# Kernel tuning notes

Measured on AMD Instinct MI355X. Metric: run time of the kernel, lower is better.

Reference implementation:

```python
import jax, jax.numpy as jnp
import numpy as np
from jax import lax

# dims
B_SZ, H_SZ, W_SZ = 2, 48, 48
D_MODEL = 192
SSM_RATIO = 2.0
D_PROJ = int(SSM_RATIO * D_MODEL)        # 384
C_INNER = 2 * D_PROJ                     # 768 = K * D_IN
K_GRP = 4
D_IN = C_INNER // K_GRP                  # 192 (= d_inner, channel_divide=2)
N_STATE = 16
R_RANK = 12                              # ceil(192/16)


def setup_inputs() -> dict:
    key = jax.random.key(0)
    ks = jax.random.split(key, 12)
    x = jax.random.normal(ks[0], (B_SZ, H_SZ, W_SZ, 2 * D_MODEL), jnp.float32)
    in_proj_w = jax.random.normal(ks[1], (C_INNER, 2 * D_MODEL), jnp.float32) * 0.02
    conv_w = jax.random.normal(ks[2], (C_INNER, 1, 3, 3), jnp.float32) * 0.1
    conv_b = jnp.zeros((C_INNER,), jnp.float32)
    x_proj_weight = jax.random.normal(ks[3], (K_GRP, R_RANK + 2 * N_STATE, D_IN), jnp.float32) * 0.05
    dt_projs_weight = jax.random.normal(ks[4], (K_GRP, D_IN, R_RANK), jnp.float32) * (R_RANK ** -0.5)
    # faithful dt bias init: softplus^{-1}(dt) with dt ~ logU[1e-3, 1e-1]
    dt = jnp.exp(jax.random.uniform(ks[5], (K_GRP, D_IN)) * (np.log(0.1) - np.log(0.001)) + np.log(0.001))
    dt = jnp.clip(dt, 1e-4, None)
    dt_projs_bias = dt + jnp.log(-jnp.expm1(-dt))
    # A_log init: log(arange(1..N)) per channel, K copies merged
    A_logs = jnp.log(jnp.tile(jnp.arange(1, N_STATE + 1, dtype=jnp.float32)[None, :], (K_GRP * D_IN, 1)))
    Ds = jnp.ones((K_GRP * D_IN,), jnp.float32)
    out_norm_w = jnp.ones((C_INNER,), jnp.float32)
    out_norm_b = jnp.zeros((C_INNER,), jnp.float32)
    out_proj_w = jax.random.normal(ks[6], (2 * D_MODEL, C_INNER), jnp.float32) * 0.02
    return dict(x=x, in_proj_w=in_proj_w, conv_w=conv_w, conv_b=conv_b,
                x_proj_weight=x_proj_weight, dt_projs_weight=dt_projs_weight,
                dt_projs_bias=dt_projs_bias, A_logs=A_logs, Ds=Ds,
                out_norm_w=out_norm_w, out_norm_b=out_norm_b, out_proj_w=out_proj_w)


def _ss2d(x, in_proj_w, conv_w, conv_b, x_proj_weight, dt_projs_weight,
          dt_projs_bias, A_logs, Ds, out_norm_w, out_norm_b, out_proj_w):
    B, H, W, _ = x.shape
    C = in_proj_w.shape[0]
    K = x_proj_weight.shape[0]
    d = C // K
    N = A_logs.shape[1]
    R = dt_projs_weight.shape[2]
    L = H * W

    # in_proj (disable_z: no gating split)
    xz = jnp.einsum('bhwc,oc->bhwo', x, in_proj_w)
    xc = xz.transpose(0, 3, 1, 2)  # [B,C,H,W]
    # depthwise 3x3 conv + SiLU
    xc = lax.conv_general_dilated(xc, conv_w, (1, 1), 'SAME', feature_group_count=C)
    xc = xc + conv_b[None, :, None, None]
    xc = xc * jax.nn.sigmoid(xc)

    # CrossScanS: split channels into K groups, each scanned in its own direction
    ch = xc.reshape(B, K, d, H, W)
    f0 = ch[:, 0].reshape(B, d, L)                                        # row-major fwd
    f1 = ch[:, 1].transpose(0, 1, 3, 2).reshape(B, d, L)                  # col-major fwd
    f2 = jnp.flip(ch[:, 2].reshape(B, d, L), -1)                          # row-major rev
    f3 = jnp.flip(ch[:, 3].transpose(0, 1, 3, 2).reshape(B, d, L), -1)    # col-major rev
    xs = jnp.stack([f0, f1, f2, f3], axis=1)  # [B,K,d,L]

    # input-dependent dt/B/C projections
    x_dbl = jnp.einsum('bkdl,kcd->bkcl', xs, x_proj_weight)
    dts, Bs, Cs = jnp.split(x_dbl, [R, R + N], axis=2)  # [B,K,R,L],[B,K,N,L],[B,K,N,L]
    dts = jnp.einsum('bkrl,kdr->bkdl', dts, dt_projs_weight) + dt_projs_bias[None, :, :, None]

    # force_fp32 selective scan with delta_softplus
    u = xs.astype(jnp.float32)
    dts = jax.nn.softplus(dts.astype(jnp.float32))
    Bs = Bs.astype(jnp.float32)
    Cs = Cs.astype(jnp.float32)
    A = -jnp.exp(A_logs.astype(jnp.float32)).reshape(K, d, N)  # [K,d,N]

    def step(h, inp):
        u_t, dt_t, B_t, C_t = inp  # [B,K,d],[B,K,d],[B,K,N],[B,K,N]
        h = h * jnp.exp(dt_t[..., None] * A) + (dt_t * u_t)[..., None] * B_t[:, :, None, :]
        y_t = jnp.einsum('bkdn,bkn->bkd', h, C_t)
        return h, y_t

    inps = (u.transpose(3, 0, 1, 2), dts.transpose(3, 0, 1, 2),
            Bs.transpose(3, 0, 1, 2), Cs.transpose(3, 0, 1, 2))
    h0 = jnp.zeros((B, K, d, N), jnp.float32)
    _, ys = lax.scan(step, h0, inps)          # ys: [L,B,K,d]
    ys = ys.transpose(1, 2, 3, 0)             # [B,K,d,L]
    ys = ys + Ds.astype(jnp.float32).reshape(K, d)[None, :, :, None] * u

    # CrossMergeS: undo each direction, concat channels back
    y0 = ys[:, 0]
    y1 = ys[:, 1].reshape(B, d, W, H).transpose(0, 1, 3, 2).reshape(B, d, L)
    y2 = jnp.flip(ys[:, 2], -1)
    y3 = jnp.flip(ys[:, 3], -1).reshape(B, d, W, H).transpose(0, 1, 3, 2).reshape(B, d, L)
    y = jnp.concatenate([y0, y1, y2, y3], axis=1).reshape(B, C, H, W).transpose(0, 2, 3, 1)

    # out_norm: LayerNorm over channels
    mu = jnp.mean(y, -1, keepdims=True)
    var = jnp.mean(jnp.square(y - mu), -1, keepdims=True)
    y = (y - mu) * lax.rsqrt(var + 1e-5) * out_norm_w + out_norm_b

    out = jnp.einsum('bhwc,oc->bhwo', y.astype(x.dtype), out_proj_w)
    return out


def reference(x, in_proj_w, conv_w, conv_b, x_proj_weight, dt_projs_weight,
              dt_projs_bias, A_logs, Ds, out_norm_w, out_norm_b, out_proj_w):
    return _ss2d(x, in_proj_w, conv_w, conv_b, x_proj_weight, dt_projs_weight,
                 dt_projs_bias, A_logs, Ds, out_norm_w, out_norm_b, out_proj_w)
```

## Files before the change

kernel.cpp:

```cpp
#include <hip/hip_runtime.h>
#include <hip/hip_bf16.h>

#define B_SZ   2
#define H_SZ   48
#define W_SZ   48
#define L_SZ   2304
#define CIN    768
#define KG     4
#define DI     192
#define NS     16
#define RR     12
#define XD     44
#define MTOK   4608
#define CL     16
#define NC     144

typedef __attribute__((ext_vector_type(8))) short short8;
typedef __attribute__((ext_vector_type(4))) float f32x4;

__device__ inline ushort f2b(float f) {
    uint u = __builtin_bit_cast(uint, f);
    u = (u + 0x7FFF + ((u >> 16) & 1)) >> 16;
    return (ushort)u;
}
__device__ inline float b2f(ushort b) {
    uint u = ((uint)b) << 16;
    return __builtin_bit_cast(float, u);
}
__device__ inline short8 f2b8(float4 a, float4 b) {
    short8 r;
    r[0] = (short)f2b(a.x); r[1] = (short)f2b(a.y);
    r[2] = (short)f2b(a.z); r[3] = (short)f2b(a.w);
    r[4] = (short)f2b(b.x); r[5] = (short)f2b(b.y);
    r[6] = (short)f2b(b.z); r[7] = (short)f2b(b.w);
    return r;
}

template<int TM, bool ABF, bool CBF>
__global__ __launch_bounds__(256) void gemm_tn64(
        const void* __restrict__ Av, const float* __restrict__ Bw,
        void* __restrict__ Cv, int M, int N, int K) {
    __shared__ ushort As[TM][40];
    __shared__ ushort Bs[64][40];
    const int tid  = threadIdx.x;
    const int lane = tid & 63;
    const int wave = tid >> 6;
    constexpr int MF = TM / 64;
    const int wrow = wave * (MF * 16);
    const int bm = blockIdx.y * TM, bn = blockIdx.x * 64;
    const int frow = lane & 15;
    const int fk   = (lane >> 4) * 8;
    const int orow = (lane >> 4) * 4;

    f32x4 acc[MF][4] = {};

    for (int k0 = 0; k0 < K; k0 += 32) {
        short8 aval[MF];
#pragma unroll
        for (int i = 0; i < MF; ++i) {
            int idx = tid + i * 256;
            int row = idx >> 2, q = idx & 3;
            if (ABF) {
                aval[i] = *(const short8*)&((const ushort*)Av)[(size_t)(bm + row) * K + k0 + q * 8];
            } else {
                const float* ap = &((const float*)Av)[(size_t)(bm + row) * K + k0 + q * 8];
                aval[i] = f2b8(*(const float4*)ap, *(const float4*)(ap + 4));
            }
        }
        const float* bp = &Bw[(size_t)(bn + (tid >> 2)) * K + k0 + (tid & 3) * 8];
        short8 bval = f2b8(*(const float4*)bp, *(const float4*)(bp + 4));

        __syncthreads();
#pragma unroll
        for (int i = 0; i < MF; ++i) {
            int idx = tid + i * 256;
            *(short8*)&As[idx >> 2][(idx & 3) * 8] = aval[i];
        }
        *(short8*)&Bs[tid >> 2][(tid & 3) * 8] = bval;
        __syncthreads();

        short8 af[MF], bf[4];
#pragma unroll
        for (int mi = 0; mi < MF; ++mi)
            af[mi] = *(const short8*)&As[wrow + mi * 16 + frow][fk];
#pragma unroll
        for (int ni = 0; ni < 4; ++ni)
            bf[ni] = *(const short8*)&Bs[ni * 16 + frow][fk];
#pragma unroll
        for (int mi = 0; mi < MF; ++mi)
#pragma unroll
            for (int ni = 0; ni < 4; ++ni)
                acc[mi][ni] = __builtin_amdgcn_mfma_f32_16x16x32_bf16(
                                  af[mi], bf[ni], acc[mi][ni], 0, 0, 0);
    }

#pragma unroll
    for (int mi = 0; mi < MF; ++mi) {
        int rbase = bm + wrow + mi * 16 + orow;
#pragma unroll
        for (int ni = 0; ni < 4; ++ni) {
            int col = bn + ni * 16 + frow;
#pragma unroll
            for (int r = 0; r < 4; ++r) {
                if (CBF)
                    ((ushort*)Cv)[(size_t)(rbase + r) * N + col] = f2b(acc[mi][ni][r]);
                else
                    ((float*)Cv)[(size_t)(rbase + r) * N + col] = acc[mi][ni][r];
            }
        }
    }
}

__global__ __launch_bounds__(256) void conv_silu_scatter(
        const ushort* __restrict__ xzb, const float* __restrict__ cw,
        const float* __restrict__ cb, ushort* __restrict__ xsb) {
    int idx = blockIdx.x * 256 + threadIdx.x;
    int c = idx % CIN;
    int rest = idx / CIN;
    int w = rest % W_SZ; rest /= W_SZ;
    int h = rest % H_SZ;
    int b = rest / H_SZ;

    float acc = cb[c];
#pragma unroll
    for (int dh = -1; dh <= 1; ++dh) {
        int hh = h + dh;
        if (hh < 0 || hh >= H_SZ) continue;
#pragma unroll
        for (int dw = -1; dw <= 1; ++dw) {
            int ww = w + dw;
            if (ww < 0 || ww >= W_SZ) continue;
            acc += b2f(xzb[(size_t)((b * H_SZ + hh) * W_SZ + ww) * CIN + c])
                 * cw[c * 9 + (dh + 1) * 3 + (dw + 1)];
        }
    }
    float s = acc * __builtin_amdgcn_rcpf(1.f + __expf(-acc));

    int k = c / DI, d = c % DI;
    int lrow = h * W_SZ + w;
    int lcol = w * H_SZ + h;
    int l;
    if      (k == 0) l = lrow;
    else if (k == 1) l = lcol;
    else if (k == 2) l = L_SZ - 1 - lrow;
    else             l = L_SZ - 1 - lcol;
    xsb[(size_t)((b * KG + k) * L_SZ + l) * DI + d] = f2b(s);
}

__global__ __launch_bounds__(384) void xproj_dt_mfma(
        const ushort* __restrict__ xsb, const float* __restrict__ xpw,
        const float* __restrict__ dtw, const float* __restrict__ dtb,
        float* __restrict__ xdbl, ushort* __restrict__ dts_b) {
    __shared__ ushort Ws[48][200];
    __shared__ ushort Wd[192][40];
    __shared__ ushort dsh[32][40];

    const int tid  = threadIdx.x;
    const int lane = tid & 63;
    const int wave = tid >> 6;
    const int bm = blockIdx.x * 32;
    const int bk = blockIdx.y;
    const int k  = bk & 3;
    const int frow = lane & 15;
    const int fk   = (lane >> 4) * 8;
    const int orow = (lane >> 4) * 4;
    const int rg = wave & 1;
    const int cg = wave >> 1;

#pragma unroll
    for (int i = 0; i < 6; ++i) {
        int idx = tid + i * 384;
        int row = idx / 48, g = idx % 48;
        ushort4 u = {0, 0, 0, 0};
        if (row < XD) {
            float4 v = *(const float4*)&xpw[((size_t)(k * XD) + row) * 192 + g * 4];
            u.x = f2b(v.x); u.y = f2b(v.y); u.z = f2b(v.z); u.w = f2b(v.w);
        }
        *(ushort4*)&Ws[row][g * 4] = u;
    }
#pragma unroll
    for (int i = 0; i < 3; ++i) {
        int idx = tid + i * 384;
        if (idx < 960) {
            float4 z = {0.f, 0.f, 0.f, 0.f};
            *(float4*)&Wd[idx / 5][(idx % 5) * 8] = z;
        } else if (idx < 1120) {
            int j = idx - 960;
            float4 z = {0.f, 0.f, 0.f, 0.f};
            *(float4*)&dsh[j / 5][(j % 5) * 8] = z;
        }
    }
    __syncthreads();

#pragma unroll
    for (int i = 0; i < 6; ++i) {
        int idx = tid + i * 384;
        int row = idx / RR, c = idx % RR;
        Wd[row][c] = f2b(dtw[((size_t)(k * DI) + row) * RR + c]);
    }

    f32x4 acc1 = {};
    const ushort* arow = &xsb[(size_t)(bk * L_SZ + bm + rg * 16 + frow) * DI];
#pragma unroll
    for (int k0 = 0; k0 < 192; k0 += 32) {
        short8 af = *(const short8*)&arow[k0 + fk];
        short8 bv = *(const short8*)&Ws[cg * 16 + frow][k0 + fk];
        acc1 = __builtin_amdgcn_mfma_f32_16x16x32_bf16(af, bv, acc1, 0, 0, 0);
    }

    {
        int col = cg * 16 + frow;
#pragma unroll
        for (int r = 0; r < 4; ++r) {
            float v = acc1[r];
            int row = rg * 16 + orow + r;
            if (col >= RR && col < XD)
                xdbl[(size_t)(bk * L_SZ + bm + row) * XD + col] = v;
            if (cg == 0 && col < RR)
                dsh[row][col] = f2b(v);
        }
    }
    __syncthreads();

#pragma unroll
    for (int t = 0; t < 2; ++t) {
        int d = (wave * 2 + t) * 16 + frow;
        short8 bv = *(const short8*)&Wd[d][fk];
        float bias = dtb[k * DI + d];
#pragma unroll
        for (int rg2 = 0; rg2 < 2; ++rg2) {
            short8 af2 = *(const short8*)&dsh[rg2 * 16 + frow][fk];
            f32x4 a2 = {};
            a2 = __builtin_amdgcn_mfma_f32_16x16x32_bf16(af2, bv, a2, 0, 0, 0);
#pragma unroll
            for (int r = 0; r < 4; ++r) {
                float a = a2[r] + bias;
                float sp = fmaxf(a, 0.f) + __logf(1.f + __expf(-fabsf(a)));
                dts_b[(size_t)(bk * L_SZ + bm + rg2 * 16 + orow + r) * DI + d] = f2b(sp);
            }
        }
    }
}

__global__ __launch_bounds__(192) void scan_passA(
        const ushort* __restrict__ dts_b, const ushort* __restrict__ xsb,
        const float* __restrict__ xdbl, const float* __restrict__ A_logs,
        float* __restrict__ Ebuf, float* __restrict__ Sbuf) {
    int blk = blockIdx.x;
    int bk = blk / NC, ch = blk % NC;
    int d = threadIdx.x, k = bk % KG;
    int l0 = ch * CL;

    __shared__ float bsh[CL][NS];
    for (int t = threadIdx.x; t < CL * NS; t += 192) {
        int l = t / NS, n = t % NS;
        bsh[l][n] = xdbl[(size_t)(bk * L_SZ + l0 + l) * XD + RR + n];
    }
    __syncthreads();

    float Aa[NS], E[NS], S[NS];
    const float* ar = &A_logs[(size_t)(k * DI + d) * NS];
    bool fast = true;
#pragma unroll
    for (int n = 0; n < NS; ++n) {
        Aa[n] = -__expf(ar[n]);
        E[n] = 1.f; S[n] = 0.f;
        fast = fast && (fabsf(Aa[n] + (float)(n + 1)) < 1e-4f * (n + 1));
    }

    if (fast) {
        float P = 1.f;
#pragma unroll 4
        for (int l = 0; l < CL; ++l) {
            float dt = b2f(dts_b[(size_t)(bk * L_SZ + l0 + l) * DI + d]);
            float u  = b2f(xsb [(size_t)(bk * L_SZ + l0 + l) * DI + d]);
            float du = dt * u;
            float4 b0 = *(const float4*)&bsh[l][0];
            float4 b1 = *(const float4*)&bsh[l][4];
            float4 b2 = *(const float4*)&bsh[l][8];
            float4 b3 = *(const float4*)&bsh[l][12];
            float Bv[NS] = {b0.x,b0.y,b0.z,b0.w, b1.x,b1.y,b1.z,b1.w,
                            b2.x,b2.y,b2.z,b2.w, b3.x,b3.y,b3.z,b3.w};
            float e1 = __expf(-dt);
            P *= e1;
            float e = e1;
            S[0] = fmaf(S[0], e, du * Bv[0]);
#pragma unroll
            for (int n = 1; n < NS; ++n) {
                e *= e1;
                S[n] = fmaf(S[n], e, du * Bv[n]);
            }
        }
        E[0] = P;
#pragma unroll
        for (int n = 1; n < NS; ++n) E[n] = E[n - 1] * P;
    } else {
#pragma unroll 4
        for (int l = 0; l < CL; ++l) {
            float dt = b2f(dts_b[(size_t)(bk * L_SZ + l0 + l) * DI + d]);
            float u  = b2f(xsb [(size_t)(bk * L_SZ + l0 + l) * DI + d]);
            float du = dt * u;
            float4 b0 = *(const float4*)&bsh[l][0];
            float4 b1 = *(const float4*)&bsh[l][4];
            float4 b2 = *(const float4*)&bsh[l][8];
            float4 b3 = *(const float4*)&bsh[l][12];
            float Bv[NS] = {b0.x,b0.y,b0.z,b0.w, b1.x,b1.y,b1.z,b1.w,
                            b2.x,b2.y,b2.z,b2.w, b3.x,b3.y,b3.z,b3.w};
#pragma unroll
            for (int n = 0; n < NS; ++n) {
                float e = __expf(dt * Aa[n]);
                E[n] *= e;
                S[n] = fmaf(S[n], e, du * Bv[n]);
            }
        }
    }
    float* ep = &Ebuf[(size_t)((bk * NC + ch) * DI + d) * NS];
    float* sp = &Sbuf[(size_t)((bk * NC + ch) * DI + d) * NS];
#pragma unroll
    for (int n = 0; n < NS; ++n) { ep[n] = E[n]; sp[n] = S[n]; }
}

__global__ __launch_bounds__(64) void scan_passB(
        const float* __restrict__ Ebuf, const float* __restrict__ Sbuf,
        float* __restrict__ Hstart) {
    constexpr int P = 8;
    int t = blockIdx.x * 64 + threadIdx.x;
    int bk = t / (DI * 4);
    int dn = (t % (DI * 4)) * 4;
    const size_t stride = (size_t)DI * NS;
    size_t off  = (size_t)(bk * NC) * stride + dn;
    size_t offL = off;

    float4 eA[P], sA[P], eB[P], sB[P];
    float4 h = {0.f, 0.f, 0.f, 0.f};

#pragma unroll
    for (int j = 0; j < P; ++j) {
        eA[j] = *(const float4*)&Ebuf[offL + (size_t)j * stride];
        sA[j] = *(const float4*)&Sbuf[offL + (size_t)j * stride];
    }
    offL += (size_t)P * stride;

    for (int c = 0; c < NC; c += 2 * P) {
#pragma unroll
        for (int j = 0; j < P; ++j) {
            eB[j] = *(const float4*)&Ebuf[offL + (size_t)j * stride];
            sB[j] = *(const float4*)&Sbuf[offL + (size_t)j * stride];
        }
        offL += (size_t)P * stride;

#pragma unroll
        for (int j = 0; j < P; ++j) {
            *(float4*)&Hstart[off + (size_t)j * stride] = h;
            h.x = fmaf(eA[j].x, h.x, sA[j].x);
            h.y = fmaf(eA[j].y, h.y, sA[j].y);
            h.z = fmaf(eA[j].z, h.z, sA[j].z);
            h.w = fmaf(eA[j].w, h.w, sA[j].w);
        }
        off += (size_t)P * stride;

        if (c + 2 * P < NC) {
#pragma unroll
            for (int j = 0; j < P; ++j) {
                eA[j] = *(const float4*)&Ebuf[offL + (size_t)j * stride];
                sA[j] = *(const float4*)&Sbuf[offL + (size_t)j * stride];
            }
        }
        offL += (size_t)P * stride;

#pragma unroll
        for (int j = 0; j < P; ++j) {
            *(float4*)&Hstart[off + (size_t)j * stride] = h;
            h.x = fmaf(eB[j].x, h.x, sB[j].x);
            h.y = fmaf(eB[j].y, h.y, sB[j].y);
            h.z = fmaf(eB[j].z, h.z, sB[j].z);
            h.w = fmaf(eB[j].w, h.w, sB[j].w);
        }
        off += (size_t)P * stride;
    }
}

__global__ __launch_bounds__(192) void scan_passC(
        const ushort* __restrict__ dts_b, const ushort* __restrict__ xsb,
        const float* __restrict__ xdbl, const float* __restrict__ A_logs,
        const float* __restrict__ Hstart, const float* __restrict__ Ds,
        ushort* __restrict__ ypre_b) {
    int blk = blockIdx.x;
    int bk = blk / NC, ch = blk % NC;
    int d = threadIdx.x, k = bk % KG, b = bk / KG;
    int l0 = ch * CL;

    __shared__ float bsh[CL][NS];
    __shared__ float csh[CL][NS];
    for (int t = threadIdx.x; t < CL * NS; t += 192) {
        int l = t / NS, n = t % NS;
        const float* row = &xdbl[(size_t)(bk * L_SZ + l0 + l) * XD];
        bsh[l][n] = row[RR + n];
        csh[l][n] = row[RR + NS + n];
    }
    __syncthreads();

    float Aa[NS], h[NS];
    const float* ar = &A_logs[(size_t)(k * DI + d) * NS];
    const float* hp = &Hstart[(size_t)((bk * NC + ch) * DI + d) * NS];
    bool fast = true;
#pragma unroll
    for (int n = 0; n < NS; ++n) {
        Aa[n] = -__expf(ar[n]);
        h[n] = hp[n];
        fast = fast && (fabsf(Aa[n] + (float)(n + 1)) < 1e-4f * (n + 1));
    }
    float Dd = Ds[k * DI + d];

#pragma unroll 4
    for (int l = 0; l < CL; ++l) {
        float dt = b2f(dts_b[(size_t)(bk * L_SZ + l0 + l) * DI + d]);
        float u  = b2f(xsb [(size_t)(bk * L_SZ + l0 + l) * DI + d]);
        float du = dt * u;
        float4 b0 = *(const float4*)&bsh[l][0];
        float4 b1 = *(const float4*)&bsh[l][4];
        float4 b2 = *(const float4*)&bsh[l][8];
        float4 b3 = *(const float4*)&bsh[l][12];
        float Bv[NS] = {b0.x,b0.y,b0.z,b0.w, b1.x,b1.y,b1.z,b1.w,
                        b2.x,b2.y,b2.z,b2.w, b3.x,b3.y,b3.z,b3.w};
        float4 c0 = *(const float4*)&csh[l][0];
        float4 c1 = *(const float4*)&csh[l][4];
        float4 c2 = *(const float4*)&csh[l][8];
        float4 c3 = *(const float4*)&csh[l][12];
        float Cv[NS] = {c0.x,c0.y,c0.z,c0.w, c1.x,c1.y,c1.z,c1.w,
                        c2.x,c2.y,c2.z,c2.w, c3.x,c3.y,c3.z,c3.w};
        float p[NS];
        if (fast) {
            float e1 = __expf(-dt);
            float e = e1;
            h[0] = fmaf(h[0], e, du * Bv[0]);
            p[0] = h[0] * Cv[0];
#pragma unroll
            for (int n = 1; n < NS; ++n) {
                e *= e1;
                h[n] = fmaf(h[n], e, du * Bv[n]);
                p[n] = h[n] * Cv[n];
            }
        } else {
#pragma unroll
            for (int n = 0; n < NS; ++n) {
                float e = __expf(dt * Aa[n]);
                h[n] = fmaf(h[n], e, du * Bv[n]);
                p[n] = h[n] * Cv[n];
            }
        }
#pragma unroll
        for (int s = 8; s >= 1; s >>= 1)
#pragma unroll
            for (int n = 0; n < 8; ++n)
                if (n < s) p[n] = p[n] + p[n + s];
        float y = fmaf(Dd, u, p[0]);

        int lg = l0 + l;
        int pos;
        if      (k == 0) pos = lg;
        else if (k == 1) pos = (lg % H_SZ) * W_SZ + (lg / H_SZ);
        else if (k == 2) pos = L_SZ - 1 - lg;
        else { int j = L_SZ - 1 - lg; pos = (j % H_SZ) * W_SZ + (j / H_SZ); }
        ypre_b[(size_t)(b * L_SZ + pos) * CIN + k * DI + d] = f2b(y);
    }
}

__global__ __launch_bounds__(256) void layernorm_bf16(
        const ushort* __restrict__ y, ushort* __restrict__ yb,
        const float* __restrict__ w, const float* __restrict__ bg) {
    int wave = threadIdx.x >> 6, lane = threadIdx.x & 63;
    int tok = blockIdx.x * 4 + wave;
    const ushort* row = &y[(size_t)tok * CIN];
    ushort* rowo = &yb[(size_t)tok * CIN];
    float v[12];
    float s = 0.f;
#pragma unroll
    for (int i = 0; i < 12; ++i) { v[i] = b2f(row[lane + i * 64]); s += v[i]; }
#pragma unroll
    for (int off = 32; off >= 1; off >>= 1) s += __shfl_xor(s, off, 64);
    float mu = s * (1.f / CIN);
    float s2 = 0.f;
#pragma unroll
    for (int i = 0; i < 12; ++i) { float t = v[i] - mu; s2 += t * t; }
#pragma unroll
    for (int off = 32; off >= 1; off >>= 1) s2 += __shfl_xor(s2, off, 64);
    float rstd = rsqrtf(s2 * (1.f / CIN) + 1e-5f);
#pragma unroll
    for (int i = 0; i < 12; ++i)
        rowo[lane + i * 64] =
            f2b((v[i] - mu) * rstd * w[lane + i * 64] + bg[lane + i * 64]);
}

extern "C" void kernel_launch(void* const* d_in, const int* in_sizes, int n_in,
                              void* d_out, int out_size, void* d_ws, size_t ws_size,
                              hipStream_t stream) {
    const float* x    = (const float*)d_in[0];
    const float* inw  = (const float*)d_in[1];
    const float* cw   = (const float*)d_in[2];
    const float* cb   = (const float*)d_in[3];
    const float* xpw  = (const float*)d_in[4];
    const float* dtw  = (const float*)d_in[5];
    const float* dtb  = (const float*)d_in[6];
    const float* alog = (const float*)d_in[7];
    const float* Dsp  = (const float*)d_in[8];
    const float* lnw  = (const float*)d_in[9];
    const float* lnb  = (const float*)d_in[10];
    const float* outw = (const float*)d_in[11];
    float* out = (float*)d_out;

    float* ws = (float*)d_ws;
    const size_t SZ_BIG = (size_t)MTOK * CIN;
    const size_t SCAN_SL = (size_t)8 * NC * DI * NS;
    float* xz    = ws;
    float* xsbf  = xz  + SZ_BIG;
    float* dts   = xsbf + SZ_BIG / 2;
    float* xdbl  = dts + SZ_BIG;
    float* Ebuf  = xdbl + (size_t)8 * L_SZ * XD;
    float* Sbuf  = Ebuf + SCAN_SL;
    float* Hst   = Sbuf + SCAN_SL;
    ushort* xzb    = (ushort*)xz;
    ushort* xsb    = (ushort*)xsbf;
    ushort* dtsb   = (ushort*)dts;
    ushort* ypre_b = (ushort*)xz;
    ushort* ynrm_b = (ushort*)dts;

    gemm_tn64<128, false, true><<<dim3(CIN / 64, MTOK / 128), 256, 0, stream>>>(
        x, inw, xzb, MTOK, CIN, 384);
    conv_silu_scatter<<<(B_SZ * H_SZ * W_SZ * CIN) / 256, 256, 0, stream>>>(xzb, cw, cb, xsb);
    xproj_dt_mfma<<<dim3(L_SZ / 32, 8), 384, 0, stream>>>(xsb, xpw, dtw, dtb, xdbl, dtsb);
    scan_passA<<<8 * NC, 192, 0, stream>>>(dtsb, xsb, xdbl, alog, Ebuf, Sbuf);
    scan_passB<<<(8 * DI * 4) / 64, 64, 0, stream>>>(Ebuf, Sbuf, Hst);
    scan_passC<<<8 * NC, 192, 0, stream>>>(dtsb, xsb, xdbl, alog, Hst, Dsp, ypre_b);
    layernorm_bf16<<<MTOK / 4, 256, 0, stream>>>(ypre_b, ynrm_b, lnw, lnb);
    gemm_tn64<64, true, false><<<dim3(384 / 64, MTOK / 64), 256, 0, stream>>>(
        ynrm_b, outw, out, MTOK, 384, CIN);
}
```

Measured before the change: 197.7 us.

## Vectorize conv over 8 channels and pass scalar chunk decay to scan carry

The depthwise conv kernel now has each thread handle 8 channels, using 16-byte loads of the input and 16-byte stores of the scattered output. The scan chunk pass A no longer writes a per-state decay array on the fast path (A = -(n+1)). It writes one scalar product per channel, and pass B rebuilds the powers from it, which cuts Ebuf write and read traffic. A few unroll factors also grow, at some cost in register pressure.

```diff
diff --git a/kernel.cpp b/kernel.cpp
--- a/kernel.cpp
+++ b/kernel.cpp
@@ -114,14 +114,26 @@
 __global__ __launch_bounds__(256) void conv_silu_scatter(
         const ushort* __restrict__ xzb, const float* __restrict__ cw,
         const float* __restrict__ cb, ushort* __restrict__ xsb) {
-    int idx = blockIdx.x * 256 + threadIdx.x;
-    int c = idx % CIN;
-    int rest = idx / CIN;
-    int w = rest % W_SZ; rest /= W_SZ;
-    int h = rest % H_SZ;
-    int b = rest / H_SZ;
-
-    float acc = cb[c];
+    int g = blockIdx.x * 256 + threadIdx.x;
+    int c8 = g % 96;
+    int pos = g / 96;
+    int w = pos % W_SZ;
+    int h = (pos / W_SZ) % H_SZ;
+    int b = pos / (W_SZ * H_SZ);
+    int c0 = c8 * 8;
+
+    float wt[72];
+    const float* cwp = &cw[c0 * 9];
+#pragma unroll
+    for (int i = 0; i < 18; ++i) {
+        float4 v = *(const float4*)(cwp + i * 4);
+        wt[i * 4 + 0] = v.x; wt[i * 4 + 1] = v.y;
+        wt[i * 4 + 2] = v.z; wt[i * 4 + 3] = v.w;
+    }
+    float acc[8];
+#pragma unroll
+    for (int j = 0; j < 8; ++j) acc[j] = cb[c0 + j];
+
 #pragma unroll
     for (int dh = -1; dh <= 1; ++dh) {
         int hh = h + dh;
@@ -130,13 +142,20 @@
         for (int dw = -1; dw <= 1; ++dw) {
             int ww = w + dw;
             if (ww < 0 || ww >= W_SZ) continue;
-            acc += b2f(xzb[(size_t)((b * H_SZ + hh) * W_SZ + ww) * CIN + c])
-                 * cw[c * 9 + (dh + 1) * 3 + (dw + 1)];
-        }
-    }
-    float s = acc * __builtin_amdgcn_rcpf(1.f + __expf(-acc));
-
-    int k = c / DI, d = c % DI;
+            int tap = (dh + 1) * 3 + (dw + 1);
+            short8 xv = *(const short8*)&xzb[(size_t)((b * H_SZ + hh) * W_SZ + ww) * CIN + c0];
+#pragma unroll
+            for (int j = 0; j < 8; ++j)
+                acc[j] = fmaf(b2f((ushort)xv[j]), wt[j * 9 + tap], acc[j]);
+        }
+    }
+
+    float s[8];
+#pragma unroll
+    for (int j = 0; j < 8; ++j)
+        s[j] = acc[j] * __builtin_amdgcn_rcpf(1.f + __expf(-acc[j]));
+
+    int k = c0 / DI, d = c0 % DI;
     int lrow = h * W_SZ + w;
     int lcol = w * H_SZ + h;
     int l;
@@ -144,7 +163,8 @@
     else if (k == 1) l = lcol;
     else if (k == 2) l = L_SZ - 1 - lrow;
     else             l = L_SZ - 1 - lcol;
-    xsb[(size_t)((b * KG + k) * L_SZ + l) * DI + d] = f2b(s);
+    float4 lo = {s[0], s[1], s[2], s[3]}, hi = {s[4], s[5], s[6], s[7]};
+    *(short8*)&xsb[(size_t)((b * KG + k) * L_SZ + l) * DI + d] = f2b8(lo, hi);
 }
 
 __global__ __launch_bounds__(384) void xproj_dt_mfma(
@@ -245,7 +265,8 @@
 __global__ __launch_bounds__(192) void scan_passA(
         const ushort* __restrict__ dts_b, const ushort* __restrict__ xsb,
         const float* __restrict__ xdbl, const float* __restrict__ A_logs,
-        float* __restrict__ Ebuf, float* __restrict__ Sbuf) {
+        float* __restrict__ Ebuf, float* __restrict__ Sbuf,
+        float* __restrict__ Pbuf) {
     int blk = blockIdx.x;
     int bk = blk / NC, ch = blk % NC;
     int d = threadIdx.x, k = bk % KG;
@@ -258,19 +279,20 @@
     }
     __syncthreads();
 
-    float Aa[NS], E[NS], S[NS];
+    float Aa[NS], S[NS];
     const float* ar = &A_logs[(size_t)(k * DI + d) * NS];
     bool fast = true;
 #pragma unroll
     for (int n = 0; n < NS; ++n) {
         Aa[n] = -__expf(ar[n]);
-        E[n] = 1.f; S[n] = 0.f;
+        S[n] = 0.f;
         fast = fast && (fabsf(Aa[n] + (float)(n + 1)) < 1e-4f * (n + 1));
     }
 
+    float* sp = &Sbuf[(size_t)((bk * NC + ch) * DI + d) * NS];
     if (fast) {
         float P = 1.f;
-#pragma unroll 4
+#pragma unroll
         for (int l = 0; l < CL; ++l) {
             float dt = b2f(dts_b[(size_t)(bk * L_SZ + l0 + l) * DI + d]);
             float u  = b2f(xsb [(size_t)(bk * L_SZ + l0 + l) * DI + d]);
@@ -291,11 +313,17 @@
                 S[n] = fmaf(S[n], e, du * Bv[n]);
             }
         }
-        E[0] = P;
-#pragma unroll
-        for (int n = 1; n < NS; ++n) E[n] = E[n - 1] * P;
+        Pbuf[(size_t)(bk * NC + ch) * DI + d] = P;
+#pragma unroll
+        for (int q = 0; q < 4; ++q) {
+            float4 v = {S[q*4], S[q*4+1], S[q*4+2], S[q*4+3]};
+            *(float4*)&sp[q * 4] = v;
+        }
     } else {
-#pragma unroll 4
+        float E[NS];
+#pragma unroll
+        for (int n = 0; n < NS; ++n) E[n] = 1.f;
+#pragma unroll 8
         for (int l = 0; l < CL; ++l) {
             float dt = b2f(dts_b[(size_t)(bk * L_SZ + l0 + l) * DI + d]);
             float u  = b2f(xsb [(size_t)(bk * L_SZ + l0 + l) * DI + d]);
@@ -313,70 +341,138 @@
                 S[n] = fmaf(S[n], e, du * Bv[n]);
             }
         }
-    }
-    float* ep = &Ebuf[(size_t)((bk * NC + ch) * DI + d) * NS];
-    float* sp = &Sbuf[(size_t)((bk * NC + ch) * DI + d) * NS];
-#pragma unroll
-    for (int n = 0; n < NS; ++n) { ep[n] = E[n]; sp[n] = S[n]; }
+        Pbuf[(size_t)(bk * NC + ch) * DI + d] = -1.f;
+        float* ep = &Ebuf[(size_t)((bk * NC + ch) * DI + d) * NS];
+#pragma unroll
+        for (int q = 0; q < 4; ++q) {
+            float4 ve = {E[q*4], E[q*4+1], E[q*4+2], E[q*4+3]};
+            float4 vs = {S[q*4], S[q*4+1], S[q*4+2], S[q*4+3]};
+            *(float4*)&ep[q * 4] = ve;
+            *(float4*)&sp[q * 4] = vs;
+        }
+    }
 }
 
 __global__ __launch_bounds__(64) void scan_passB(
         const float* __restrict__ Ebuf, const float* __restrict__ Sbuf,
-        float* __restrict__ Hstart) {
+        const float* __restrict__ Pbuf, float* __restrict__ Hstart) {
     constexpr int P = 8;
     int t = blockIdx.x * 64 + threadIdx.x;
     int bk = t / (DI * 4);
     int dn = (t % (DI * 4)) * 4;
+    int d  = dn >> 4;
+    int n0 = dn & 15;
     const size_t stride = (size_t)DI * NS;
     size_t off  = (size_t)(bk * NC) * stride + dn;
-    size_t offL = off;
-
-    float4 eA[P], sA[P], eB[P], sB[P];
+    const float* pb = &Pbuf[(size_t)(bk * NC) * DI + d];
+
     float4 h = {0.f, 0.f, 0.f, 0.f};
-
-#pragma unroll
-    for (int j = 0; j < P; ++j) {
-        eA[j] = *(const float4*)&Ebuf[offL + (size_t)j * stride];
-        sA[j] = *(const float4*)&Sbuf[offL + (size_t)j * stride];
-    }
-    offL += (size_t)P * stride;
-
-    for (int c = 0; c < NC; c += 2 * P) {
+    bool fastu = (pb[0] >= 0.f);
+
+    if (fastu) {
+        float  pA[P], pB[P];
+        float4 sA[P], sB[P];
+        size_t offL = off;
+        int    cP   = 0;
 #pragma unroll
         for (int j = 0; j < P; ++j) {
-            eB[j] = *(const float4*)&Ebuf[offL + (size_t)j * stride];
-            sB[j] = *(const float4*)&Sbuf[offL + (size_t)j * stride];
+            pA[j] = pb[(size_t)(cP + j) * DI];
+            sA[j] = *(const float4*)&Sbuf[offL + (size_t)j * stride];
+        }
+        offL += (size_t)P * stride; cP += P;
+
+        for (int c = 0; c < NC; c += 2 * P) {
+#pragma unroll
+            for (int j = 0; j < P; ++j) {
+                pB[j] = pb[(size_t)(cP + j) * DI];
+                sB[j] = *(const float4*)&Sbuf[offL + (size_t)j * stride];
+            }
+            offL += (size_t)P * stride; cP += P;
+
+#pragma unroll
+            for (int j = 0; j < P; ++j) {
+                *(float4*)&Hstart[off + (size_t)j * stride] = h;
+                float Pv = pA[j];
+                float P2 = Pv * Pv, P3 = P2 * Pv;
+                float P4 = P2 * P2, P8 = P4 * P4;
+                float base = Pv * ((n0 & 4) ? P4 : 1.f) * ((n0 & 8) ? P8 : 1.f);
+                h.x = fmaf(base,      h.x, sA[j].x);
+                h.y = fmaf(base * Pv, h.y, sA[j].y);
+                h.z = fmaf(base * P2, h.z, sA[j].z);
+                h.w = fmaf(base * P3, h.w, sA[j].w);
+            }
+            off += (size_t)P * stride;
+
+            if (c + 2 * P < NC) {
+#pragma unroll
+                for (int j = 0; j < P; ++j) {
+                    pA[j] = pb[(size_t)(cP + j) * DI];
+                    sA[j] = *(const float4*)&Sbuf[offL + (size_t)j * stride];
+                }
+            }
+            offL += (size_t)P * stride; cP += P;
+
+#pragma unroll
+            for (int j = 0; j < P; ++j) {
+                *(float4*)&Hstart[off + (size_t)j * stride] = h;
+                float Pv = pB[j];
+                float P2 = Pv * Pv, P3 = P2 * Pv;
+                float P4 = P2 * P2, P8 = P4 * P4;
+                float base = Pv * ((n0 & 4) ? P4 : 1.f) * ((n0 & 8) ? P8 : 1.f);
+                h.x = fmaf(base,      h.x, sB[j].x);
+                h.y = fmaf(base * Pv, h.y, sB[j].y);
+                h.z = fmaf(base * P2, h.z, sB[j].z);
+                h.w = fmaf(base * P3, h.w, sB[j].w);
+            }
+            off += (size_t)P * stride;
+        }
+    } else {
+        float4 eA[P], sA[P], eB[P], sB[P];
+        size_t offL = off;
+#pragma unroll
+        for (int j = 0; j < P; ++j) {
+            eA[j] = *(const float4*)&Ebuf[offL + (size_t)j * stride];
+            sA[j] = *(const float4*)&Sbuf[offL + (size_t)j * stride];
         }
         offL += (size_t)P * stride;
 
-#pragma unroll
-        for (int j = 0; j < P; ++j) {
-            *(float4*)&Hstart[off + (size_t)j * stride] = h;
-            h.x = fmaf(eA[j].x, h.x, sA[j].x);
-            h.y = fmaf(eA[j].y, h.y, sA[j].y);
-            h.z = fmaf(eA[j].z, h.z, sA[j].z);
-            h.w = fmaf(eA[j].w, h.w, sA[j].w);
-        }
-        off += (size_t)P * stride;
-
-        if (c + 2 * P < NC) {
+        for (int c = 0; c < NC; c += 2 * P) {
 #pragma unroll
             for (int j = 0; j < P; ++j) {
-                eA[j] = *(const float4*)&Ebuf[offL + (size_t)j * stride];
-                sA[j] = *(const float4*)&Sbuf[offL + (size_t)j * stride];
-            }
-        }
-        offL += (size_t)P * stride;
-
-#pragma unroll
-        for (int j = 0; j < P; ++j) {
-            *(float4*)&Hstart[off + (size_t)j * stride] = h;
-            h.x = fmaf(eB[j].x, h.x, sB[j].x);
-            h.y = fmaf(eB[j].y, h.y, sB[j].y);
-            h.z = fmaf(eB[j].z, h.z, sB[j].z);
-            h.w = fmaf(eB[j].w, h.w, sB[j].w);
-        }
-        off += (size_t)P * stride;
+                eB[j] = *(const float4*)&Ebuf[offL + (size_t)j * stride];
+                sB[j] = *(const float4*)&Sbuf[offL + (size_t)j * stride];
+            }
+            offL += (size_t)P * stride;
+
+#pragma unroll
+            for (int j = 0; j < P; ++j) {
+                *(float4*)&Hstart[off + (size_t)j * stride] = h;
+                h.x = fmaf(eA[j].x, h.x, sA[j].x);
+                h.y = fmaf(eA[j].y, h.y, sA[j].y);
+                h.z = fmaf(eA[j].z, h.z, sA[j].z);
+                h.w = fmaf(eA[j].w, h.w, sA[j].w);
+            }
+            off += (size_t)P * stride;
+
+            if (c + 2 * P < NC) {
+#pragma unroll
+                for (int j = 0; j < P; ++j) {
+                    eA[j] = *(const float4*)&Ebuf[offL + (size_t)j * stride];
+                    sA[j] = *(const float4*)&Sbuf[offL + (size_t)j * stride];
+                }
+            }
+            offL += (size_t)P * stride;
+
+#pragma unroll
+            for (int j = 0; j < P; ++j) {
+                *(float4*)&Hstart[off + (size_t)j * stride] = h;
+                h.x = fmaf(eB[j].x, h.x, sB[j].x);
+                h.y = fmaf(eB[j].y, h.y, sB[j].y);
+                h.z = fmaf(eB[j].z, h.z, sB[j].z);
+                h.w = fmaf(eB[j].w, h.w, sB[j].w);
+            }
+            off += (size_t)P * stride;
+        }
     }
 }
 
@@ -412,7 +508,7 @@
     }
     float Dd = Ds[k * DI + d];
 
-#pragma unroll 4
+#pragma unroll 8
     for (int l = 0; l < CL; ++l) {
         float dt = b2f(dts_b[(size_t)(bk * L_SZ + l0 + l) * DI + d]);
         float u  = b2f(xsb [(size_t)(bk * L_SZ + l0 + l) * DI + d]);
@@ -519,6 +615,7 @@
     float* Ebuf  = xdbl + (size_t)8 * L_SZ * XD;
     float* Sbuf  = Ebuf + SCAN_SL;
     float* Hst   = Sbuf + SCAN_SL;
+    float* Pbuf  = Hst + SCAN_SL;
     ushort* xzb    = (ushort*)xz;
     ushort* xsb    = (ushort*)xsbf;
     ushort* dtsb   = (ushort*)dts;
@@ -527,10 +624,10 @@
 
     gemm_tn64<128, false, true><<<dim3(CIN / 64, MTOK / 128), 256, 0, stream>>>(
         x, inw, xzb, MTOK, CIN, 384);
-    conv_silu_scatter<<<(B_SZ * H_SZ * W_SZ * CIN) / 256, 256, 0, stream>>>(xzb, cw, cb, xsb);
+    conv_silu_scatter<<<(B_SZ * H_SZ * W_SZ * 96) / 256, 256, 0, stream>>>(xzb, cw, cb, xsb);
     xproj_dt_mfma<<<dim3(L_SZ / 32, 8), 384, 0, stream>>>(xsb, xpw, dtw, dtb, xdbl, dtsb);
-    scan_passA<<<8 * NC, 192, 0, stream>>>(dtsb, xsb, xdbl, alog, Ebuf, Sbuf);
-    scan_passB<<<(8 * DI * 4) / 64, 64, 0, stream>>>(Ebuf, Sbuf, Hst);
+    scan_passA<<<8 * NC, 192, 0, stream>>>(dtsb, xsb, xdbl, alog, Ebuf, Sbuf, Pbuf);
+    scan_passB<<<(8 * DI * 4) / 64, 64, 0, stream>>>(Ebuf, Sbuf, Pbuf, Hst);
     scan_passC<<<8 * NC, 192, 0, stream>>>(dtsb, xsb, xdbl, alog, Hst, Dsp, ypre_b);
     layernorm_bf16<<<MTOK / 4, 256, 0, stream>>>(ypre_b, ynrm_b, lnw, lnb);
     gemm_tn64<64, true, false><<<dim3(384 / 64, MTOK / 64), 256, 0, stream>>>(
```

Result: faster. 184.6 us (-6.6%).
